# Kernel tuning notes

Measured on AMD Instinct MI355X. Metric: run time of the kernel, lower is better.

The kernel has to match this reference:

```python
import jax, jax.numpy as jnp
import numpy as np

N = 50000    # nodes
E = 640000   # edges (avg degree ~12.8)
D = 128      # feature dim (input = hidden = output)
L = 3        # num_layers
BN_EPS = 1e-5


def setup_inputs() -> dict:
    key = jax.random.key(0)
    ks = jax.random.split(key, 6)
    x = jax.random.normal(ks[0], (N, D), dtype=jnp.float32)
    edge_index = jax.random.randint(ks[1], (2, E), 0, N, dtype=jnp.int32)
    s = 1.0 / np.sqrt(D)
    # Weights stored as (in, out); equivalent to torch Linear's x @ W.T with W:(out,in).
    W1 = jax.random.normal(ks[2], (L, D, D), dtype=jnp.float32) * s
    b1 = jnp.zeros((L, D), dtype=jnp.float32)
    gamma = jnp.ones((L, D), dtype=jnp.float32)   # BatchNorm weight
    beta = jnp.zeros((L, D), dtype=jnp.float32)   # BatchNorm bias
    W2 = jax.random.normal(ks[3], (L, D, D), dtype=jnp.float32) * s
    b2 = jnp.zeros((L, D), dtype=jnp.float32)
    return {"x": x, "W1": W1, "b1": b1, "gamma": gamma, "beta": beta,
            "W2": W2, "b2": b2, "edge_index": edge_index}


def reference(x, W1, b1, gamma, beta, W2, b2, edge_index):
    src = edge_index[0]
    dst = edge_index[1]
    h = x
    for i in range(L):
        # GINConv aggregation: sum of source-node features into destinations, eps=0
        agg = jax.ops.segment_sum(h[src], dst, num_segments=N)   # [N, D]
        z = h + agg                                              # (1+eps)*x + sum_j x_j
        # MLP: Linear -> BatchNorm1d (training stats) -> ReLU -> Linear
        z = z @ W1[i] + b1[i]
        mu = jnp.mean(z, axis=0)
        var = jnp.mean((z - mu) ** 2, axis=0)                    # biased var (torch BN)
        z = (z - mu) * jax.lax.rsqrt(var + BN_EPS) * gamma[i] + beta[i]
        z = jax.nn.relu(z)
        z = z @ W2[i] + b2[i]
        # inter-layer ReLU (dropout_rate=0 -> identity)
        h = jax.nn.relu(z) if i < L - 1 else z
    return h
```

## Files before the change

kernel.cpp:

```cpp
#include <hip/hip_runtime.h>

#define D 128
#define BN_EPS 1e-5f
#define ELLW 64

typedef __bf16 bf16_t;
typedef __bf16 bf16x8 __attribute__((ext_vector_type(8)));
typedef __bf16 bf16x4 __attribute__((ext_vector_type(4)));
typedef __bf16 bf16x2 __attribute__((ext_vector_type(2)));
typedef float floatx4 __attribute__((ext_vector_type(4)));

__global__ void prep(const float* __restrict__ x, bf16_t* __restrict__ hb,
                     const float* __restrict__ W1, const float* __restrict__ W2,
                     bf16_t* __restrict__ Wsw, int* __restrict__ deg,
                     float* __restrict__ stats, int N, int n4) {
  int i = blockIdx.x * blockDim.x + threadIdx.x;
  if (i < n4) {
    float4 v = ((const float4*)x)[i];
    bf16x4 p;
    p[0] = (bf16_t)v.x; p[1] = (bf16_t)v.y; p[2] = (bf16_t)v.z; p[3] = (bf16_t)v.w;
    *(bf16x4*)(hb + (size_t)4 * i) = p;
  }
  if (i < N) deg[i] = 0;
  if (i < 768) stats[i] = 0.f;
  if (i < 6 * 16384) {
    int mat = i >> 14;
    int kn = i & 16383;
    int k = kn >> 7;
    int n = kn & 127;
    const float* Wm = (mat < 3) ? (W1 + (size_t)mat * 16384)
                                : (W2 + (size_t)(mat - 3) * 16384);
    float v = Wm[kn];
    int f = ((n >> 4) << 2) | (k >> 5);
    int ln = (((k >> 3) & 3) << 4) | (n & 15);
    int j = k & 7;
    Wsw[(size_t)mat * 16384 + ((f << 6) + ln) * 8 + j] = (bf16_t)v;
  }
}

__global__ void ell_fill(const int* __restrict__ src, const int* __restrict__ dst,
                         int* __restrict__ deg, int* __restrict__ ell, int E) {
  int e = blockIdx.x * blockDim.x + threadIdx.x;
  if (e < E) {
    int d = dst[e];
    int slot = atomicAdd(&deg[d], 1);
    if (slot < ELLW) ell[(size_t)d * ELLW + slot] = src[e];
  }
}

__global__ __launch_bounds__(256) void aggregate(
    const bf16_t* __restrict__ h, bf16_t* __restrict__ z,
    const int* __restrict__ ell, const int* __restrict__ deg, int Nn) {
  int node = blockIdx.x * 4 + (threadIdx.x >> 6);
  if (node >= Nn) return;
  int lane = threadIdx.x & 63;
  int off = lane << 1;
  int dg = deg[node]; if (dg > ELLW) dg = ELLW;
  const int* nb = ell + (size_t)node * ELLW;

  bf16x2 sv = *(const bf16x2*)(h + (size_t)node * D + off);
  float a0x = (float)sv[0], a0y = (float)sv[1];
  float a1x = 0.f, a1y = 0.f, a2x = 0.f, a2y = 0.f, a3x = 0.f, a3y = 0.f;
  int e = 0;
  for (; e + 8 <= dg; e += 8) {
    int4 ia = *(const int4*)(nb + e);
    int4 ib = *(const int4*)(nb + e + 4);
    bf16x2 v0 = *(const bf16x2*)(h + (size_t)ia.x * D + off);
    bf16x2 v1 = *(const bf16x2*)(h + (size_t)ia.y * D + off);
    bf16x2 v2 = *(const bf16x2*)(h + (size_t)ia.z * D + off);
    bf16x2 v3 = *(const bf16x2*)(h + (size_t)ia.w * D + off);
    bf16x2 v4 = *(const bf16x2*)(h + (size_t)ib.x * D + off);
    bf16x2 v5 = *(const bf16x2*)(h + (size_t)ib.y * D + off);
    bf16x2 v6 = *(const bf16x2*)(h + (size_t)ib.z * D + off);
    bf16x2 v7 = *(const bf16x2*)(h + (size_t)ib.w * D + off);
    a0x += (float)v0[0]; a0y += (float)v0[1];
    a1x += (float)v1[0]; a1y += (float)v1[1];
    a2x += (float)v2[0]; a2y += (float)v2[1];
    a3x += (float)v3[0]; a3y += (float)v3[1];
    a0x += (float)v4[0]; a0y += (float)v4[1];
    a1x += (float)v5[0]; a1y += (float)v5[1];
    a2x += (float)v6[0]; a2y += (float)v6[1];
    a3x += (float)v7[0]; a3y += (float)v7[1];
  }
  for (; e + 4 <= dg; e += 4) {
    int4 i4 = *(const int4*)(nb + e);
    bf16x2 v0 = *(const bf16x2*)(h + (size_t)i4.x * D + off);
    bf16x2 v1 = *(const bf16x2*)(h + (size_t)i4.y * D + off);
    bf16x2 v2 = *(const bf16x2*)(h + (size_t)i4.z * D + off);
    bf16x2 v3 = *(const bf16x2*)(h + (size_t)i4.w * D + off);
    a0x += (float)v0[0]; a0y += (float)v0[1];
    a1x += (float)v1[0]; a1y += (float)v1[1];
    a2x += (float)v2[0]; a2y += (float)v2[1];
    a3x += (float)v3[0]; a3y += (float)v3[1];
  }
  for (; e < dg; ++e) {
    bf16x2 v = *(const bf16x2*)(h + (size_t)nb[e] * D + off);
    a0x += (float)v[0]; a0y += (float)v[1];
  }
  a0x += a1x + a2x + a3x;
  a0y += a1y + a2y + a3y;
  bf16x2 o;
  o[0] = (bf16_t)a0x; o[1] = (bf16_t)a0y;
  *(bf16x2*)(z + (size_t)node * D + off) = o;
}

__global__ __launch_bounds__(256) void gemm1_stats(
    const bf16_t* __restrict__ Z, const bf16_t* __restrict__ Wsw1,
    const float* __restrict__ bias1, float* __restrict__ stats,
    int nStrips, int N) {
  __shared__ float sred[256];
  const int t = threadIdx.x;
  const int lane = t & 63;
  const int l15 = lane & 15;
  const int quad = lane >> 4;
  const int strip = blockIdx.x * 4 + (t >> 6);
  const bool active = strip < nStrips;

  sred[t] = 0.f;
  __syncthreads();

  bf16x8 a[4];
  const int row = strip * 16 + l15;
  if (active && row < N) {
#pragma unroll
    for (int kc = 0; kc < 4; ++kc)
      a[kc] = *(const bf16x8*)(Z + (size_t)row * D + kc * 32 + quad * 8);
  } else {
#pragma unroll
    for (int kc = 0; kc < 4; ++kc)
#pragma unroll
      for (int j = 0; j < 8; ++j) a[kc][j] = (bf16_t)0.f;
  }

  floatx4 acc[8];
#pragma unroll
  for (int nt = 0; nt < 8; ++nt) {
    float bv = bias1[nt * 16 + l15];
    acc[nt] = (floatx4){bv, bv, bv, bv};
  }
#pragma unroll
  for (int nt = 0; nt < 8; ++nt) {
#pragma unroll
    for (int kc = 0; kc < 4; ++kc) {
      bf16x8 b = *(const bf16x8*)(Wsw1 + (size_t)((nt * 4 + kc) * 64 + lane) * 8);
      acc[nt] = __builtin_amdgcn_mfma_f32_16x16x32_bf16(a[kc], b, acc[nt], 0, 0, 0);
    }
  }

  const int rowBase = strip * 16 + quad * 4;
#pragma unroll
  for (int nt = 0; nt < 8; ++nt) {
    int c = nt * 16 + l15;
    float s = 0.f, q = 0.f;
    if (active) {
#pragma unroll
      for (int r = 0; r < 4; ++r) {
        if (rowBase + r < N) {
          float v = acc[nt][r];
          s += v; q += v * v;
        }
      }
    }
    s += __shfl_xor(s, 16); s += __shfl_xor(s, 32);
    q += __shfl_xor(q, 16); q += __shfl_xor(q, 32);
    if (quad == 0) {
      atomicAdd(&sred[c], s);
      atomicAdd(&sred[128 + c], q);
    }
  }
  __syncthreads();
  atomicAdd(&stats[t], sred[t]);
}

__global__ __launch_bounds__(256) void mlp2r(
    const bf16_t* __restrict__ Z, const float* __restrict__ stats,
    const float* __restrict__ gamma, const float* __restrict__ beta,
    const bf16_t* __restrict__ Wsw1, const float* __restrict__ bias1,
    const bf16_t* __restrict__ Wsw2, const float* __restrict__ bias2,
    void* __restrict__ outp, int nStrips, int N, float invN,
    int relu_out, int fp32_out) {
  __shared__ bf16_t T[64][136];
  __shared__ float abL[256];
  const int t = threadIdx.x;
  const int wv = t >> 6;
  const int lane = t & 63;
  const int l15 = lane & 15;
  const int quad = lane >> 4;
  const int strip = blockIdx.x * 4 + wv;
  const bool active = strip < nStrips;

  if (t < 128) {
    float mu = stats[t] * invN;
    float var = fmaxf(stats[128 + t] * invN - mu * mu, 0.f);
    float ai = gamma[t] * rsqrtf(var + BN_EPS);
    abL[t] = ai;
    abL[128 + t] = beta[t] - mu * ai;
  }

  bf16x8 a[4];
  const int row = strip * 16 + l15;
  if (active && row < N) {
#pragma unroll
    for (int kc = 0; kc < 4; ++kc)
      a[kc] = *(const bf16x8*)(Z + (size_t)row * D + kc * 32 + quad * 8);
  } else {
#pragma unroll
    for (int kc = 0; kc < 4; ++kc)
#pragma unroll
      for (int j = 0; j < 8; ++j) a[kc][j] = (bf16_t)0.f;
  }

  floatx4 acc[8];
#pragma unroll
  for (int nt = 0; nt < 8; ++nt) {
    float bv = bias1[nt * 16 + l15];
    acc[nt] = (floatx4){bv, bv, bv, bv};
  }
#pragma unroll
  for (int nt = 0; nt < 8; ++nt) {
#pragma unroll
    for (int kc = 0; kc < 4; ++kc) {
      bf16x8 b = *(const bf16x8*)(Wsw1 + (size_t)((nt * 4 + kc) * 64 + lane) * 8);
      acc[nt] = __builtin_amdgcn_mfma_f32_16x16x32_bf16(a[kc], b, acc[nt], 0, 0, 0);
    }
  }

  __syncthreads();

  float bnA[8], bnB[8];
#pragma unroll
  for (int nt = 0; nt < 8; ++nt) {
    int c = nt * 16 + l15;
    bnA[nt] = abL[c];
    bnB[nt] = abL[128 + c];
  }

  const int lr = wv * 16 + quad * 4;
#pragma unroll
  for (int nt = 0; nt < 8; ++nt) {
    int c = nt * 16 + l15;
#pragma unroll
    for (int r = 0; r < 4; ++r)
      T[lr + r][c] = (bf16_t)fmaxf(fmaf(acc[nt][r], bnA[nt], bnB[nt]), 0.f);
  }
  __syncthreads();

  bf16x8 a2[4];
#pragma unroll
  for (int kc = 0; kc < 4; ++kc)
    a2[kc] = *(const bf16x8*)&T[wv * 16 + l15][kc * 32 + quad * 8];

#pragma unroll
  for (int nt = 0; nt < 8; ++nt) {
    float bv = bias2[nt * 16 + l15];
    acc[nt] = (floatx4){bv, bv, bv, bv};
  }
#pragma unroll
  for (int nt = 0; nt < 8; ++nt) {
#pragma unroll
    for (int kc = 0; kc < 4; ++kc) {
      bf16x8 b = *(const bf16x8*)(Wsw2 + (size_t)((nt * 4 + kc) * 64 + lane) * 8);
      acc[nt] = __builtin_amdgcn_mfma_f32_16x16x32_bf16(a2[kc], b, acc[nt], 0, 0, 0);
    }
  }

  if (!active) return;
  const int rowBase = strip * 16 + quad * 4;
  if (fp32_out) {
    float* out = (float*)outp;
#pragma unroll
    for (int nt = 0; nt < 8; ++nt) {
      int c = nt * 16 + l15;
#pragma unroll
      for (int r = 0; r < 4; ++r) {
        int rw = rowBase + r;
        if (rw < N) {
          float v = acc[nt][r];
          if (relu_out) v = fmaxf(v, 0.f);
          out[(size_t)rw * D + c] = v;
        }
      }
    }
  } else {
    bf16_t* out = (bf16_t*)outp;
#pragma unroll
    for (int nt = 0; nt < 8; ++nt) {
      int c = nt * 16 + l15;
#pragma unroll
      for (int r = 0; r < 4; ++r) {
        int rw = rowBase + r;
        if (rw < N) {
          float v = acc[nt][r];
          if (relu_out) v = fmaxf(v, 0.f);
          out[(size_t)rw * D + c] = (bf16_t)v;
        }
      }
    }
  }
}

extern "C" void kernel_launch(void* const* d_in, const int* in_sizes, int n_in,
                              void* d_out, int out_size, void* d_ws, size_t ws_size,
                              hipStream_t stream) {
  const float* x     = (const float*)d_in[0];
  const float* W1    = (const float*)d_in[1];
  const float* b1    = (const float*)d_in[2];
  const float* gamma = (const float*)d_in[3];
  const float* beta  = (const float*)d_in[4];
  const float* W2    = (const float*)d_in[5];
  const float* b2    = (const float*)d_in[6];
  const int*   ei    = (const int*)d_in[7];

  const int N = in_sizes[0] / D;
  const int E = in_sizes[7] / 2;
  const int* src = ei;
  const int* dst = ei + E;

  char* ws = (char*)d_ws;
  size_t bufBytes = (size_t)N * D * sizeof(bf16_t);
  bf16_t* hb   = (bf16_t*)ws;
  bf16_t* zb   = (bf16_t*)(ws + bufBytes);
  int*    ell  = (int*)(ws + 2 * bufBytes);
  int*    deg  = (int*)((char*)ell + (size_t)N * ELLW * sizeof(int));
  float*  stats = (float*)((char*)deg + (size_t)N * sizeof(int));
  bf16_t* Wsw  = (bf16_t*)(stats + 768);

  const int n4 = N * D / 4;
  const int prepBlocks = (n4 + 255) / 256;
  const int eb = (E + 255) / 256;
  const int aggBlocks = (N + 3) / 4;
  const int nStrips = (N + 15) / 16;
  const int gemmBlocks = (nStrips + 3) / 4;
  const float invN = 1.f / (float)N;

  prep<<<prepBlocks, 256, 0, stream>>>(x, hb, W1, W2, Wsw, deg, stats, N, n4);
  ell_fill<<<eb, 256, 0, stream>>>(src, dst, deg, ell, E);

  for (int i = 0; i < 3; ++i) {
    float* st = stats + (size_t)i * 256;
    aggregate<<<aggBlocks, 256, 0, stream>>>(hb, zb, ell, deg, N);
    gemm1_stats<<<gemmBlocks, 256, 0, stream>>>(
        zb, Wsw + (size_t)i * 16384, b1 + (size_t)i * D, st, nStrips, N);
    void* Ob = (i == 2) ? d_out : (void*)hb;
    mlp2r<<<gemmBlocks, 256, 0, stream>>>(
        zb, st, gamma + (size_t)i * D, beta + (size_t)i * D,
        Wsw + (size_t)i * 16384, b1 + (size_t)i * D,
        Wsw + (size_t)(i + 3) * 16384, b2 + (size_t)i * D,
        Ob, nStrips, N, invN, (i < 2) ? 1 : 0, (i == 2) ? 1 : 0);
  }
}
```

Measured before the change: 349.3 us.

## Widen aggregate gathers to 8-byte loads and shard BN stats atomics

The aggregate kernel now assigns 32 lanes per node, each loading 4 bf16 values (8 bytes) per neighbor instead of 2. Each wavefront therefore covers two nodes, and the 8-wide neighbor unroll is dropped. The BatchNorm statistic accumulation is spread across 8 replicated stats slots chosen by block index, which reduces contention from global atomics on the same 256 addresses. mlp2r then sums the 8 partial slots when it computes mean and variance. The trade-off is fewer loads in flight per lane, a little extra reduction work, and a larger stats buffer.

```diff
diff --git a/kernel.cpp b/kernel.cpp
--- a/kernel.cpp
+++ b/kernel.cpp
@@ -3,6 +3,7 @@
 #define D 128
 #define BN_EPS 1e-5f
 #define ELLW 64
+#define SGRP 8
 
 typedef __bf16 bf16_t;
 typedef __bf16 bf16x8 __attribute__((ext_vector_type(8)));
@@ -22,7 +23,7 @@
     *(bf16x4*)(hb + (size_t)4 * i) = p;
   }
   if (i < N) deg[i] = 0;
-  if (i < 768) stats[i] = 0.f;
+  if (i < 3 * SGRP * 256) stats[i] = 0.f;
   if (i < 6 * 16384) {
     int mat = i >> 14;
     int kn = i & 16383;
@@ -51,57 +52,44 @@
 __global__ __launch_bounds__(256) void aggregate(
     const bf16_t* __restrict__ h, bf16_t* __restrict__ z,
     const int* __restrict__ ell, const int* __restrict__ deg, int Nn) {
-  int node = blockIdx.x * 4 + (threadIdx.x >> 6);
+  int node = blockIdx.x * 8 + (threadIdx.x >> 5);
   if (node >= Nn) return;
-  int lane = threadIdx.x & 63;
-  int off = lane << 1;
+  int s = threadIdx.x & 31;
+  int off = s << 2;
   int dg = deg[node]; if (dg > ELLW) dg = ELLW;
   const int* nb = ell + (size_t)node * ELLW;
 
-  bf16x2 sv = *(const bf16x2*)(h + (size_t)node * D + off);
-  float a0x = (float)sv[0], a0y = (float)sv[1];
-  float a1x = 0.f, a1y = 0.f, a2x = 0.f, a2y = 0.f, a3x = 0.f, a3y = 0.f;
+  bf16x4 sv = *(const bf16x4*)(h + (size_t)node * D + off);
+  floatx4 A0 = {(float)sv[0], (float)sv[1], (float)sv[2], (float)sv[3]};
+  floatx4 A1 = {0.f, 0.f, 0.f, 0.f};
+  floatx4 A2 = {0.f, 0.f, 0.f, 0.f};
+  floatx4 A3 = {0.f, 0.f, 0.f, 0.f};
   int e = 0;
-  for (; e + 8 <= dg; e += 8) {
-    int4 ia = *(const int4*)(nb + e);
-    int4 ib = *(const int4*)(nb + e + 4);
-    bf16x2 v0 = *(const bf16x2*)(h + (size_t)ia.x * D + off);
-    bf16x2 v1 = *(const bf16x2*)(h + (size_t)ia.y * D + off);
-    bf16x2 v2 = *(const bf16x2*)(h + (size_t)ia.z * D + off);
-    bf16x2 v3 = *(const bf16x2*)(h + (size_t)ia.w * D + off);
-    bf16x2 v4 = *(const bf16x2*)(h + (size_t)ib.x * D + off);
-    bf16x2 v5 = *(const bf16x2*)(h + (size_t)ib.y * D + off);
-    bf16x2 v6 = *(const bf16x2*)(h + (size_t)ib.z * D + off);
-    bf16x2 v7 = *(const bf16x2*)(h + (size_t)ib.w * D + off);
-    a0x += (float)v0[0]; a0y += (float)v0[1];
-    a1x += (float)v1[0]; a1y += (float)v1[1];
-    a2x += (float)v2[0]; a2y += (float)v2[1];
-    a3x += (float)v3[0]; a3y += (float)v3[1];
-    a0x += (float)v4[0]; a0y += (float)v4[1];
-    a1x += (float)v5[0]; a1y += (float)v5[1];
-    a2x += (float)v6[0]; a2y += (float)v6[1];
-    a3x += (float)v7[0]; a3y += (float)v7[1];
-  }
   for (; e + 4 <= dg; e += 4) {
     int4 i4 = *(const int4*)(nb + e);
-    bf16x2 v0 = *(const bf16x2*)(h + (size_t)i4.x * D + off);
-    bf16x2 v1 = *(const bf16x2*)(h + (size_t)i4.y * D + off);
-    bf16x2 v2 = *(const bf16x2*)(h + (size_t)i4.z * D + off);
-    bf16x2 v3 = *(const bf16x2*)(h + (size_t)i4.w * D + off);
-    a0x += (float)v0[0]; a0y += (float)v0[1];
-    a1x += (float)v1[0]; a1y += (float)v1[1];
-    a2x += (float)v2[0]; a2y += (float)v2[1];
-    a3x += (float)v3[0]; a3y += (float)v3[1];
+    bf16x4 v0 = *(const bf16x4*)(h + (size_t)i4.x * D + off);
+    bf16x4 v1 = *(const bf16x4*)(h + (size_t)i4.y * D + off);
+    bf16x4 v2 = *(const bf16x4*)(h + (size_t)i4.z * D + off);
+    bf16x4 v3 = *(const bf16x4*)(h + (size_t)i4.w * D + off);
+#pragma unroll
+    for (int j = 0; j < 4; ++j) {
+      A0[j] += (float)v0[j];
+      A1[j] += (float)v1[j];
+      A2[j] += (float)v2[j];
+      A3[j] += (float)v3[j];
+    }
   }
   for (; e < dg; ++e) {
-    bf16x2 v = *(const bf16x2*)(h + (size_t)nb[e] * D + off);
-    a0x += (float)v[0]; a0y += (float)v[1];
-  }
-  a0x += a1x + a2x + a3x;
-  a0y += a1y + a2y + a3y;
-  bf16x2 o;
-  o[0] = (bf16_t)a0x; o[1] = (bf16_t)a0y;
-  *(bf16x2*)(z + (size_t)node * D + off) = o;
+    bf16x4 v = *(const bf16x4*)(h + (size_t)nb[e] * D + off);
+#pragma unroll
+    for (int j = 0; j < 4; ++j) A0[j] += (float)v[j];
+  }
+#pragma unroll
+  for (int j = 0; j < 4; ++j) A0[j] += A1[j] + A2[j] + A3[j];
+  bf16x4 o;
+  o[0] = (bf16_t)A0[0]; o[1] = (bf16_t)A0[1];
+  o[2] = (bf16_t)A0[2]; o[3] = (bf16_t)A0[3];
+  *(bf16x4*)(z + (size_t)node * D + off) = o;
 }
 
 __global__ __launch_bounds__(256) void gemm1_stats(
@@ -169,7 +157,7 @@
     }
   }
   __syncthreads();
-  atomicAdd(&stats[t], sred[t]);
+  atomicAdd(&stats[((blockIdx.x & (SGRP - 1)) << 8) + t], sred[t]);
 }
 
 __global__ __launch_bounds__(256) void mlp2r(
@@ -190,8 +178,14 @@
   const bool active = strip < nStrips;
 
   if (t < 128) {
-    float mu = stats[t] * invN;
-    float var = fmaxf(stats[128 + t] * invN - mu * mu, 0.f);
+    float s0 = 0.f, q0 = 0.f;
+#pragma unroll
+    for (int g = 0; g < SGRP; ++g) {
+      s0 += stats[(g << 8) + t];
+      q0 += stats[(g << 8) + 128 + t];
+    }
+    float mu = s0 * invN;
+    float var = fmaxf(q0 * invN - mu * mu, 0.f);
     float ai = gamma[t] * rsqrtf(var + BN_EPS);
     abL[t] = ai;
     abL[128 + t] = beta[t] - mu * ai;
@@ -323,12 +317,12 @@
   int*    ell  = (int*)(ws + 2 * bufBytes);
   int*    deg  = (int*)((char*)ell + (size_t)N * ELLW * sizeof(int));
   float*  stats = (float*)((char*)deg + (size_t)N * sizeof(int));
-  bf16_t* Wsw  = (bf16_t*)(stats + 768);
+  bf16_t* Wsw  = (bf16_t*)(stats + 3 * SGRP * 256);
 
   const int n4 = N * D / 4;
   const int prepBlocks = (n4 + 255) / 256;
   const int eb = (E + 255) / 256;
-  const int aggBlocks = (N + 3) / 4;
+  const int aggBlocks = (N + 7) / 8;
   const int nStrips = (N + 15) / 16;
   const int gemmBlocks = (nStrips + 3) / 4;
   const float invN = 1.f / (float)N;
@@ -337,7 +331,7 @@
   ell_fill<<<eb, 256, 0, stream>>>(src, dst, deg, ell, E);
 
   for (int i = 0; i < 3; ++i) {
-    float* st = stats + (size_t)i * 256;
+    float* st = stats + (size_t)i * SGRP * 256;
     aggregate<<<aggBlocks, 256, 0, stream>>>(hb, zb, ell, deg, N);
     gemm1_stats<<<gemmBlocks, 256, 0, stream>>>(
         zb, Wsw + (size_t)i * 16384, b1 + (size_t)i * D, st, nStrips, N);
```

Result: faster. 301.3 us (-13.7%).
